# Optimization experiments

Hardware: AMD Instinct MI355X
Metric: run time of the kernel (lower is better)

Reference implementation:

```python
import jax, jax.numpy as jnp
import numpy as np

# MXFP4 e2m1 value lookup (sign bit is the high bit of the nibble)
FP4_LUT = jnp.array([0.0, 0.5, 1.0, 1.5, 2.0, 3.0, 4.0, 6.0,
                     -0.0, -0.5, -1.0, -1.5, -2.0, -3.0, -4.0, -6.0], dtype=jnp.float32)
BLOCK = 32  # mxfp4 scale block size
TOP_K = 2


def dequant_mxfp4(blocks, scales):
    # blocks: [..., K//2] packed uint8 nibbles (low nibble = even elem, high = odd)
    # scales: [..., K//BLOCK] e8m0 biased exponents; scale = 2**(s - 127)
    b = blocks.astype(jnp.int32)
    lo = b & 0xF
    hi = (b >> 4) & 0xF
    nib = jnp.stack([lo, hi], axis=-1).reshape(blocks.shape[:-1] + (blocks.shape[-1] * 2,))
    vals = FP4_LUT[nib]                                   # [..., K]
    s = jnp.exp2(scales.astype(jnp.float32) - 127.0)      # [..., K//BLOCK]
    s = jnp.repeat(s, BLOCK, axis=-1)                     # [..., K]
    return vals * s


def setup_inputs() -> dict:
    key = jax.random.key(0)
    ks = jax.random.split(key, 8)
    E, H, F, B, S = 16, 1024, 2048, 1, 128
    hidden_states = jax.random.normal(ks[0], (B, S, H), dtype=jnp.float32)
    router_w = jax.random.normal(ks[1], (E, H), dtype=jnp.float32) * 0.05
    blocks_gu = jax.random.randint(ks[2], (E, 2 * F, H // 2), 0, 256, dtype=jnp.int32)
    scales_gu = jax.random.randint(ks[3], (E, 2 * F, H // BLOCK), 118, 130, dtype=jnp.int32)
    bias_gu = jax.random.normal(ks[4], (E, 2 * F), dtype=jnp.float32) * 0.02
    blocks_down = jax.random.randint(ks[5], (E, H, F // 2), 0, 256, dtype=jnp.int32)
    scales_down = jax.random.randint(ks[6], (E, H, F // BLOCK), 118, 130, dtype=jnp.int32)
    bias_down = jax.random.normal(ks[7], (E, H), dtype=jnp.float32) * 0.02
    return {"hidden_states": hidden_states, "router_w": router_w,
            "bias_gu": bias_gu, "bias_down": bias_down,
            "blocks_gu": blocks_gu, "scales_gu": scales_gu,
            "blocks_down": blocks_down, "scales_down": scales_down}


def reference(hidden_states, router_w, bias_gu, bias_down,
              blocks_gu, scales_gu, blocks_down, scales_down):
    B, S, H = hidden_states.shape
    flat = hidden_states.reshape(-1, H)                   # [T, H]
    T = flat.shape[0]
    E = router_w.shape[0]

    # --- routing: topk_then_softmax (default softmax_order) ---
    logits = flat @ router_w.T                            # [T, E]
    top_vals, top_idx = jax.lax.top_k(logits, TOP_K)      # [T, K]
    weights = jax.nn.softmax(top_vals, axis=-1).astype(flat.dtype)
    combine = jnp.zeros((T, E), flat.dtype).at[jnp.arange(T)[:, None], top_idx].set(weights)

    # --- mxfp4 dequant of fused expert weights ---
    w_gu = dequant_mxfp4(blocks_gu, scales_gu)            # [E, 2F, H]
    w_down = dequant_mxfp4(blocks_down, scales_down)      # [E, H, F]

    # --- expert MLP (SwiGLU), combined with routing weights ---
    gu = jnp.einsum('th,eoh->eto', flat, w_gu) + bias_gu[:, None, :]   # [E, T, 2F]
    gate, up = jnp.split(gu, 2, axis=-1)
    h = jax.nn.silu(gate) * up                            # [E, T, F]
    y = jnp.einsum('etf,ehf->eth', h, w_down) + bias_down[:, None, :]  # [E, T, H]
    out = jnp.einsum('eth,te->th', y, combine)            # [T, H]
    return out.reshape(B, S, H)
```

## Files before the change

### kernel.cpp

```cpp
#include <hip/hip_runtime.h>
#include <hip/hip_fp16.h>
#include <math.h>

#define NE 16
#define HD 1024
#define FD 2048

typedef _Float16 half8 __attribute__((ext_vector_type(8)));
typedef float f32x4 __attribute__((ext_vector_type(4)));

#define TOPI_OFF 0
#define TOPW_OFF 256
#define CNT_OFF  512
#define PREF_OFF 528
#define SLOT_OFF 544
#define INVT_OFF 800
#define META_OFF 1056
#define TL1_OFF  1060
#define XH_OFF   4096
#define HBUF_OFF (XH_OFF + 131072)
#define Y_OFF    (HBUF_OFF + 262144)

union XI { int4 v; half8 h; };

__device__ __forceinline__ int fp4h(int nib) {
    int c = nib & 7;
    int v;
    if (c == 0) v = 0;
    else if (c == 1) v = 14 << 10;
    else v = (((c >> 1) + 14) << 10) | ((c & 1) << 9);
    v |= (nib & 8) << 12;
    return v;
}

__device__ __forceinline__ int dec2i(const int* lut, int byte, int sv) {
    int l = lut[byte & 255];
    __half2 p = *reinterpret_cast<const __half2*>(&l);
    __half2 sc = *reinterpret_cast<const __half2*>(&sv);
    __half2 r = __hmul2(p, sc);
    return *reinterpret_cast<int*>(&r);
}

__global__ void routing_kernel(const float* __restrict__ x, const float* __restrict__ rw,
                               int* __restrict__ top_idx, float* __restrict__ top_w) {
    int t = blockIdx.x;
    int tid = threadIdx.x;
    int e = tid >> 4, seg = tid & 15;
    const float* xr = x + t * HD + seg * 64;
    const float* wr = rw + e * HD + seg * 64;
    float p = 0.f;
    #pragma unroll 8
    for (int i = 0; i < 64; ++i) p += xr[i] * wr[i];
    __shared__ float part[16][16];
    __shared__ float logit[16];
    part[e][seg] = p;
    __syncthreads();
    if (tid < 16) {
        float s = 0.f;
        #pragma unroll
        for (int i = 0; i < 16; ++i) s += part[tid][i];
        logit[tid] = s;
    }
    __syncthreads();
    if (tid == 0) {
        int i0 = 0; float v0 = logit[0];
        #pragma unroll
        for (int i = 1; i < 16; ++i) { if (logit[i] > v0) { v0 = logit[i]; i0 = i; } }
        int i1 = -1; float v1 = -1e30f;
        #pragma unroll
        for (int i = 0; i < 16; ++i) { if (i != i0 && logit[i] > v1) { v1 = logit[i]; i1 = i; } }
        float w0 = 1.f / (1.f + expf(v1 - v0));
        float w1 = 1.f / (1.f + expf(v0 - v1));
        top_idx[t * 2]     = i0;  top_w[t * 2]     = w0;
        top_idx[t * 2 + 1] = i1;  top_w[t * 2 + 1] = w1;
    }
}

__global__ void build_kernel(const int* __restrict__ top_idx,
                             int* __restrict__ cnt, int* __restrict__ pref,
                             int* __restrict__ slot, int* __restrict__ invtok,
                             int* __restrict__ meta, int* __restrict__ tl1) {
    __shared__ int scnt[16], spref[16], scur[16];
    int tid = threadIdx.x;
    if (tid < 16) scnt[tid] = 0;
    __syncthreads();
    int e = top_idx[tid];
    atomicAdd(&scnt[e], 1);
    __syncthreads();
    if (tid == 0) {
        int s = 0;
        for (int i = 0; i < 16; ++i) { spref[i] = s; pref[i] = s; cnt[i] = scnt[i]; s += scnt[i]; }
        int m1 = 0;
        for (int i = 0; i < 16; ++i) {
            int ntile1 = (scnt[i] + 15) >> 4;
            for (int m = 0; m < ntile1; ++m) tl1[m1++] = (i << 8) | m;
        }
        meta[0] = m1;
    }
    if (tid < 16) scur[tid] = 0;
    __syncthreads();
    int pos = spref[e] + atomicAdd(&scur[e], 1);
    slot[tid] = pos;
    invtok[pos] = tid >> 1;
}

__global__ void gather_kernel(const float* __restrict__ x, const int* __restrict__ invtok,
                              _Float16* __restrict__ xh) {
    int slt = blockIdx.x;
    int t = invtok[slt];
    int i = threadIdx.x;
    float4 v = ((const float4*)(x + (long)t * HD))[i];
    union { _Float16 h[4]; int2 p; } o;
    o.h[0] = (_Float16)v.x; o.h[1] = (_Float16)v.y;
    o.h[2] = (_Float16)v.z; o.h[3] = (_Float16)v.w;
    ((int2*)(xh + (long)slt * HD))[i] = o.p;
}

__global__ __launch_bounds__(256) void gemm1_mfma(
    const _Float16* __restrict__ xh, const int* __restrict__ qblk,
    const int* __restrict__ qscl, const float* __restrict__ bias,
    const int* __restrict__ cnt, const int* __restrict__ pref,
    const int* __restrict__ meta, const int* __restrict__ tl1,
    _Float16* __restrict__ hbuf) {
    __shared__ int lut[256];
    __shared__ int4 Asb[128];
    __shared__ int4 Bsb[512];
    __shared__ float exch[4][64][4];
    int tid = threadIdx.x;
    lut[tid] = fp4h(tid & 15) | (fp4h(tid >> 4) << 16);
    int wave = tid >> 6, lane = tid & 63;
    int bl = lane & 15, kb4 = lane >> 4;
    int rloc = wave * 16 + bl;
    int rs = tid >> 2, kq = tid & 3;
    int tok = tid >> 3, ga = tid & 7;
    int nwork = meta[0] << 6;

    for (int w = blockIdx.x; w < nwork; w += gridDim.x) {
        int tile = tl1[w >> 6];
        int fc = w & 63;
        int e = tile >> 8, mt = tile & 255;
        int n = cnt[e];
        int nt = n - mt * 16; if (nt > 16) nt = 16;
        int base = pref[e];
        int t0 = base + mt * 16;
        int f0 = fc * 32;

        long rowg = (long)e * 4096 + ((rs < 32) ? (f0 + rs) : (2048 + f0 + rs - 32));
        const int4* wrow = (const int4*)(qblk + rowg * 512);
        const int* srow = qscl + rowg * 32;
        int tclamp = (tok < nt) ? tok : nt - 1;
        const int4* arow = (const int4*)xh + (long)(t0 + tclamp) * 128;

        f32x4 acc = {0.f, 0.f, 0.f, 0.f};
        for (int kb = 0; kb < 16; ++kb) {
            __syncthreads();
            if (tid < 128)
                Asb[tok * 8 + (ga ^ (tok & 7))] = arow[kb * 8 + ga];
            {
                int4 q0 = wrow[kb * 8 + kq * 2];
                int4 q1 = wrow[kb * 8 + kq * 2 + 1];
                int sc = srow[kb * 2 + (kq >> 1)];
                int sv = (sc - 112) << 10; sv |= sv << 16;
                int4 o0, o1;
                o0.x = dec2i(lut, q0.x, sv); o0.y = dec2i(lut, q0.y, sv);
                o0.z = dec2i(lut, q0.z, sv); o0.w = dec2i(lut, q0.w, sv);
                o1.x = dec2i(lut, q1.x, sv); o1.y = dec2i(lut, q1.y, sv);
                o1.z = dec2i(lut, q1.z, sv); o1.w = dec2i(lut, q1.w, sv);
                Bsb[rs * 8 + ((kq * 2) ^ (rs & 7))] = o0;
                Bsb[rs * 8 + ((kq * 2 + 1) ^ (rs & 7))] = o1;
            }
            __syncthreads();
            #pragma unroll
            for (int ks = 0; ks < 2; ++ks) {
                int g = ks * 4 + kb4;
                XI a, b;
                a.v = Asb[bl * 8 + (g ^ (bl & 7))];
                b.v = Bsb[rloc * 8 + (g ^ (rloc & 7))];
                acc = __builtin_amdgcn_mfma_f32_16x16x32_f16(a.h, b.h, acc, 0, 0, 0);
            }
        }
        #pragma unroll
        for (int i = 0; i < 4; ++i) exch[wave][lane][i] = acc[i];
        __syncthreads();
        int fl = tid & 31, wv = fl >> 4, col = fl & 15;
        float bg = bias[(long)e * 4096 + f0 + fl];
        float bu = bias[(long)e * 4096 + 2048 + f0 + fl];
        #pragma unroll
        for (int d = 0; d < 2; ++d) {
            int tk = (tid >> 5) + d * 8;
            int ln = ((tk >> 2) << 4) | col;
            int rg = tk & 3;
            float g = exch[wv][ln][rg] + bg;
            float u = exch[wv + 2][ln][rg] + bu;
            float h = (g / (1.f + expf(-g))) * u;
            if (tk < nt)
                hbuf[(long)(t0 + tk) * FD + f0 + fl] = (_Float16)(h * 0.0625f);
        }
    }
}

__global__ __launch_bounds__(256) void gemm2_mfma(
    const _Float16* __restrict__ hbuf, const int* __restrict__ qblk,
    const int* __restrict__ qscl, const float* __restrict__ bias,
    const int* __restrict__ cnt, const int* __restrict__ pref,
    const int* __restrict__ meta, const int* __restrict__ tl1,
    float* __restrict__ y) {
    __shared__ int lut[256];
    __shared__ int4 Asb[128];
    __shared__ int4 Bsb[512];
    int tid = threadIdx.x;
    lut[tid] = fp4h(tid & 15) | (fp4h(tid >> 4) << 16);
    int wave = tid >> 6, lane = tid & 63;
    int bl = lane & 15, kb4 = lane >> 4;
    int rloc = wave * 16 + bl;
    int rs = tid >> 2, kq = tid & 3;
    int tok = tid >> 3, ga = tid & 7;
    int nwork = meta[0] << 5;

    for (int w = blockIdx.x; w < nwork; w += gridDim.x) {
        int tile = tl1[w >> 5];
        int sub = w & 31;
        int hc = sub & 15, kh = sub >> 4;
        int e = tile >> 8, mt = tile & 255;
        int n = cnt[e];
        int nt = n - mt * 16; if (nt > 16) nt = 16;
        int base = pref[e];
        int t0 = base + mt * 16;
        int h0 = hc * 64;

        long rowg = (long)e * HD + h0 + rs;
        const int4* wrow = (const int4*)(qblk + rowg * 1024);
        const int* srow = qscl + rowg * 64;
        int tclamp = (tok < nt) ? tok : nt - 1;
        const int4* arow = (const int4*)hbuf + (long)(t0 + tclamp) * 256;
        int kb0 = kh * 16;

        f32x4 acc = {0.f, 0.f, 0.f, 0.f};
        for (int kb = 0; kb < 16; ++kb) {
            int kbb = kb0 + kb;
            __syncthreads();
            if (tid < 128)
                Asb[tok * 8 + (ga ^ (tok & 7))] = arow[kbb * 8 + ga];
            {
                int4 q0 = wrow[kbb * 8 + kq * 2];
                int4 q1 = wrow[kbb * 8 + kq * 2 + 1];
                int sc = srow[kbb * 2 + (kq >> 1)];
                int sv = (sc - 112) << 10; sv |= sv << 16;
                int4 o0, o1;
                o0.x = dec2i(lut, q0.x, sv); o0.y = dec2i(lut, q0.y, sv);
                o0.z = dec2i(lut, q0.z, sv); o0.w = dec2i(lut, q0.w, sv);
                o1.x = dec2i(lut, q1.x, sv); o1.y = dec2i(lut, q1.y, sv);
                o1.z = dec2i(lut, q1.z, sv); o1.w = dec2i(lut, q1.w, sv);
                Bsb[rs * 8 + ((kq * 2) ^ (rs & 7))] = o0;
                Bsb[rs * 8 + ((kq * 2 + 1) ^ (rs & 7))] = o1;
            }
            __syncthreads();
            #pragma unroll
            for (int ks = 0; ks < 2; ++ks) {
                int g = ks * 4 + kb4;
                XI a, b;
                a.v = Asb[bl * 8 + (g ^ (bl & 7))];
                b.v = Bsb[rloc * 8 + (g ^ (rloc & 7))];
                acc = __builtin_amdgcn_mfma_f32_16x16x32_f16(a.h, b.h, acc, 0, 0, 0);
            }
        }
        int hcol = h0 + wave * 16 + bl;
        float bv = (kh == 0) ? bias[(long)e * HD + hcol] : 0.f;
        #pragma unroll
        for (int r = 0; r < 4; ++r) {
            int row = kb4 * 4 + r;
            if (row < nt)
                atomicAdd(&y[(long)(t0 + row) * HD + hcol], acc[r] * 16.f + bv);
        }
    }
}

__global__ void combine_kernel(const float* __restrict__ y, const int* __restrict__ slot,
                               const float* __restrict__ topw, float* __restrict__ out) {
    int t = blockIdx.x;
    int i = threadIdx.x;
    int s0 = slot[2 * t], s1 = slot[2 * t + 1];
    float w0 = topw[2 * t], w1 = topw[2 * t + 1];
    float4 a = ((const float4*)(y + (long)s0 * HD))[i];
    float4 b = ((const float4*)(y + (long)s1 * HD))[i];
    float4 o;
    o.x = w0 * a.x + w1 * b.x;
    o.y = w0 * a.y + w1 * b.y;
    o.z = w0 * a.z + w1 * b.z;
    o.w = w0 * a.w + w1 * b.w;
    ((float4*)(out + (long)t * HD))[i] = o;
}

extern "C" void kernel_launch(void* const* d_in, const int* in_sizes, int n_in,
                              void* d_out, int out_size, void* d_ws, size_t ws_size,
                              hipStream_t stream) {
    const float* x          = (const float*)d_in[0];
    const float* rw         = (const float*)d_in[1];
    const float* bias_gu    = (const float*)d_in[2];
    const float* bias_down  = (const float*)d_in[3];
    const int*   blocks_gu  = (const int*)d_in[4];
    const int*   scales_gu  = (const int*)d_in[5];
    const int*   blocks_down= (const int*)d_in[6];
    const int*   scales_down= (const int*)d_in[7];
    float* out = (float*)d_out;
    int*   wsI = (int*)d_ws;
    float* wsF = (float*)d_ws;
    _Float16* xh   = (_Float16*)(wsI + XH_OFF);
    _Float16* hbuf = (_Float16*)(wsI + HBUF_OFF);
    float*    y    = wsF + Y_OFF;

    (void)hipMemsetAsync(y, 0, 256 * HD * sizeof(float), stream);
    routing_kernel<<<128, 256, 0, stream>>>(x, rw, wsI + TOPI_OFF, wsF + TOPW_OFF);
    build_kernel<<<1, 256, 0, stream>>>(wsI + TOPI_OFF, wsI + CNT_OFF, wsI + PREF_OFF,
                                        wsI + SLOT_OFF, wsI + INVT_OFF,
                                        wsI + META_OFF, wsI + TL1_OFF);
    gather_kernel<<<256, 256, 0, stream>>>(x, wsI + INVT_OFF, xh);
    gemm1_mfma<<<2048, 256, 0, stream>>>(xh, blocks_gu, scales_gu, bias_gu,
                                         wsI + CNT_OFF, wsI + PREF_OFF,
                                         wsI + META_OFF, wsI + TL1_OFF, hbuf);
    gemm2_mfma<<<1024, 256, 0, stream>>>(hbuf, blocks_down, scales_down, bias_down,
                                         wsI + CNT_OFF, wsI + PREF_OFF,
                                         wsI + META_OFF, wsI + TL1_OFF, y);
    combine_kernel<<<128, 256, 0, stream>>>(y, wsI + SLOT_OFF, wsF + TOPW_OFF, out);
}
```

Before: 67.93 us.

## Double-buffer LDS tiles in both GEMMs and replace atomics with split-K buffers

Both GEMM kernels now keep two shared-memory buffers. Global loads for the next K block are issued before the MFMAs on the current block, and only one barrier is left per iteration, so memory latency overlaps with compute. The gemm2 split-K halves write plain stores into two separate y buffers instead of doing atomicAdd into one. This removes the memset and the atomic traffic, at the cost of combine reading four rows per token instead of two. The added cost is twice the LDS and more registers, which may reduce occupancy.

```diff
diff --git a/kernel.cpp b/kernel.cpp
--- a/kernel.cpp
+++ b/kernel.cpp
@@ -19,7 +19,8 @@
 #define TL1_OFF  1060
 #define XH_OFF   4096
 #define HBUF_OFF (XH_OFF + 131072)
-#define Y_OFF    (HBUF_OFF + 262144)
+#define Y0_OFF   (HBUF_OFF + 262144)
+#define Y1_OFF   (Y0_OFF + 262144)
 
 union XI { int4 v; half8 h; };
 
@@ -123,8 +124,8 @@
     const int* __restrict__ meta, const int* __restrict__ tl1,
     _Float16* __restrict__ hbuf) {
     __shared__ int lut[256];
-    __shared__ int4 Asb[128];
-    __shared__ int4 Bsb[512];
+    __shared__ int4 Asb[2][128];
+    __shared__ int4 Bsb[2][512];
     __shared__ float exch[4][64][4];
     int tid = threadIdx.x;
     lut[tid] = fp4h(tid & 15) | (fp4h(tid >> 4) << 16);
@@ -151,32 +152,54 @@
         int tclamp = (tok < nt) ? tok : nt - 1;
         const int4* arow = (const int4*)xh + (long)(t0 + tclamp) * 128;
 
+        int4 q0 = wrow[kq * 2];
+        int4 q1 = wrow[kq * 2 + 1];
+        int sc = srow[kq >> 1];
+        int4 av;
+        if (tid < 128) av = arow[ga];
+        __syncthreads();
+        if (tid < 128) Asb[0][tok * 8 + (ga ^ (tok & 7))] = av;
+        {
+            int sv = (sc - 112) << 10; sv |= sv << 16;
+            int4 o0, o1;
+            o0.x = dec2i(lut, q0.x, sv); o0.y = dec2i(lut, q0.y, sv);
+            o0.z = dec2i(lut, q0.z, sv); o0.w = dec2i(lut, q0.w, sv);
+            o1.x = dec2i(lut, q1.x, sv); o1.y = dec2i(lut, q1.y, sv);
+            o1.z = dec2i(lut, q1.z, sv); o1.w = dec2i(lut, q1.w, sv);
+            Bsb[0][rs * 8 + ((kq * 2) ^ (rs & 7))] = o0;
+            Bsb[0][rs * 8 + ((kq * 2 + 1) ^ (rs & 7))] = o1;
+        }
+        __syncthreads();
+
         f32x4 acc = {0.f, 0.f, 0.f, 0.f};
         for (int kb = 0; kb < 16; ++kb) {
-            __syncthreads();
-            if (tid < 128)
-                Asb[tok * 8 + (ga ^ (tok & 7))] = arow[kb * 8 + ga];
-            {
-                int4 q0 = wrow[kb * 8 + kq * 2];
-                int4 q1 = wrow[kb * 8 + kq * 2 + 1];
-                int sc = srow[kb * 2 + (kq >> 1)];
+            int cur = kb & 1;
+            if (kb < 15) {
+                q0 = wrow[(kb + 1) * 8 + kq * 2];
+                q1 = wrow[(kb + 1) * 8 + kq * 2 + 1];
+                sc = srow[(kb + 1) * 2 + (kq >> 1)];
+                if (tid < 128) av = arow[(kb + 1) * 8 + ga];
+            }
+            #pragma unroll
+            for (int ks = 0; ks < 2; ++ks) {
+                int g = ks * 4 + kb4;
+                XI a, b;
+                a.v = Asb[cur][bl * 8 + (g ^ (bl & 7))];
+                b.v = Bsb[cur][rloc * 8 + (g ^ (rloc & 7))];
+                acc = __builtin_amdgcn_mfma_f32_16x16x32_f16(a.h, b.h, acc, 0, 0, 0);
+            }
+            if (kb < 15) {
+                int nxt = cur ^ 1;
+                if (tid < 128) Asb[nxt][tok * 8 + (ga ^ (tok & 7))] = av;
                 int sv = (sc - 112) << 10; sv |= sv << 16;
                 int4 o0, o1;
                 o0.x = dec2i(lut, q0.x, sv); o0.y = dec2i(lut, q0.y, sv);
                 o0.z = dec2i(lut, q0.z, sv); o0.w = dec2i(lut, q0.w, sv);
                 o1.x = dec2i(lut, q1.x, sv); o1.y = dec2i(lut, q1.y, sv);
                 o1.z = dec2i(lut, q1.z, sv); o1.w = dec2i(lut, q1.w, sv);
-                Bsb[rs * 8 + ((kq * 2) ^ (rs & 7))] = o0;
-                Bsb[rs * 8 + ((kq * 2 + 1) ^ (rs & 7))] = o1;
-            }
-            __syncthreads();
-            #pragma unroll
-            for (int ks = 0; ks < 2; ++ks) {
-                int g = ks * 4 + kb4;
-                XI a, b;
-                a.v = Asb[bl * 8 + (g ^ (bl & 7))];
-                b.v = Bsb[rloc * 8 + (g ^ (rloc & 7))];
-                acc = __builtin_amdgcn_mfma_f32_16x16x32_f16(a.h, b.h, acc, 0, 0, 0);
+                Bsb[nxt][rs * 8 + ((kq * 2) ^ (rs & 7))] = o0;
+                Bsb[nxt][rs * 8 + ((kq * 2 + 1) ^ (rs & 7))] = o1;
+                __syncthreads();
             }
         }
         #pragma unroll
@@ -204,10 +227,10 @@
     const int* __restrict__ qscl, const float* __restrict__ bias,
     const int* __restrict__ cnt, const int* __restrict__ pref,
     const int* __restrict__ meta, const int* __restrict__ tl1,
-    float* __restrict__ y) {
+    float* __restrict__ y0p, float* __restrict__ y1p) {
     __shared__ int lut[256];
-    __shared__ int4 Asb[128];
-    __shared__ int4 Bsb[512];
+    __shared__ int4 Asb[2][128];
+    __shared__ int4 Bsb[2][512];
     int tid = threadIdx.x;
     lut[tid] = fp4h(tid & 15) | (fp4h(tid >> 4) << 16);
     int wave = tid >> 6, lane = tid & 63;
@@ -229,65 +252,90 @@
         int h0 = hc * 64;
 
         long rowg = (long)e * HD + h0 + rs;
-        const int4* wrow = (const int4*)(qblk + rowg * 1024);
-        const int* srow = qscl + rowg * 64;
+        const int4* wrow = (const int4*)(qblk + rowg * 1024) + (kh * 16) * 8;
+        const int* srow = qscl + rowg * 64 + kh * 32;
         int tclamp = (tok < nt) ? tok : nt - 1;
-        const int4* arow = (const int4*)hbuf + (long)(t0 + tclamp) * 256;
-        int kb0 = kh * 16;
+        const int4* arow = (const int4*)hbuf + (long)(t0 + tclamp) * 256 + (kh * 16) * 8;
+
+        int4 q0 = wrow[kq * 2];
+        int4 q1 = wrow[kq * 2 + 1];
+        int sc = srow[kq >> 1];
+        int4 av;
+        if (tid < 128) av = arow[ga];
+        __syncthreads();
+        if (tid < 128) Asb[0][tok * 8 + (ga ^ (tok & 7))] = av;
+        {
+            int sv = (sc - 112) << 10; sv |= sv << 16;
+            int4 o0, o1;
+            o0.x = dec2i(lut, q0.x, sv); o0.y = dec2i(lut, q0.y, sv);
+            o0.z = dec2i(lut, q0.z, sv); o0.w = dec2i(lut, q0.w, sv);
+            o1.x = dec2i(lut, q1.x, sv); o1.y = dec2i(lut, q1.y, sv);
+            o1.z = dec2i(lut, q1.z, sv); o1.w = dec2i(lut, q1.w, sv);
+            Bsb[0][rs * 8 + ((kq * 2) ^ (rs & 7))] = o0;
+            Bsb[0][rs * 8 + ((kq * 2 + 1) ^ (rs & 7))] = o1;
+        }
+        __syncthreads();
 
         f32x4 acc = {0.f, 0.f, 0.f, 0.f};
         for (int kb = 0; kb < 16; ++kb) {
-            int kbb = kb0 + kb;
-            __syncthreads();
-            if (tid < 128)
-                Asb[tok * 8 + (ga ^ (tok & 7))] = arow[kbb * 8 + ga];
-            {
-                int4 q0 = wrow[kbb * 8 + kq * 2];
-                int4 q1 = wrow[kbb * 8 + kq * 2 + 1];
-                int sc = srow[kbb * 2 + (kq >> 1)];
+            int cur = kb & 1;
+            if (kb < 15) {
+                q0 = wrow[(kb + 1) * 8 + kq * 2];
+                q1 = wrow[(kb + 1) * 8 + kq * 2 + 1];
+                sc = srow[(kb + 1) * 2 + (kq >> 1)];
+                if (tid < 128) av = arow[(kb + 1) * 8 + ga];
+            }
+            #pragma unroll
+            for (int ks = 0; ks < 2; ++ks) {
+                int g = ks * 4 + kb4;
+                XI a, b;
+                a.v = Asb[cur][bl * 8 + (g ^ (bl & 7))];
+                b.v = Bsb[cur][rloc * 8 + (g ^ (rloc & 7))];
+                acc = __builtin_amdgcn_mfma_f32_16x16x32_f16(a.h, b.h, acc, 0, 0, 0);
+            }
+            if (kb < 15) {
+                int nxt = cur ^ 1;
+                if (tid < 128) Asb[nxt][tok * 8 + (ga ^ (tok & 7))] = av;
                 int sv = (sc - 112) << 10; sv |= sv << 16;
                 int4 o0, o1;
                 o0.x = dec2i(lut, q0.x, sv); o0.y = dec2i(lut, q0.y, sv);
                 o0.z = dec2i(lut, q0.z, sv); o0.w = dec2i(lut, q0.w, sv);
                 o1.x = dec2i(lut, q1.x, sv); o1.y = dec2i(lut, q1.y, sv);
                 o1.z = dec2i(lut, q1.z, sv); o1.w = dec2i(lut, q1.w, sv);
-                Bsb[rs * 8 + ((kq * 2) ^ (rs & 7))] = o0;
-                Bsb[rs * 8 + ((kq * 2 + 1) ^ (rs & 7))] = o1;
-            }
-            __syncthreads();
-            #pragma unroll
-            for (int ks = 0; ks < 2; ++ks) {
-                int g = ks * 4 + kb4;
-                XI a, b;
-                a.v = Asb[bl * 8 + (g ^ (bl & 7))];
-                b.v = Bsb[rloc * 8 + (g ^ (rloc & 7))];
-                acc = __builtin_amdgcn_mfma_f32_16x16x32_f16(a.h, b.h, acc, 0, 0, 0);
+                Bsb[nxt][rs * 8 + ((kq * 2) ^ (rs & 7))] = o0;
+                Bsb[nxt][rs * 8 + ((kq * 2 + 1) ^ (rs & 7))] = o1;
+                __syncthreads();
             }
         }
         int hcol = h0 + wave * 16 + bl;
         float bv = (kh == 0) ? bias[(long)e * HD + hcol] : 0.f;
+        float* yp = (kh == 0) ? y0p : y1p;
         #pragma unroll
         for (int r = 0; r < 4; ++r) {
             int row = kb4 * 4 + r;
             if (row < nt)
-                atomicAdd(&y[(long)(t0 + row) * HD + hcol], acc[r] * 16.f + bv);
-        }
-    }
-}
-
-__global__ void combine_kernel(const float* __restrict__ y, const int* __restrict__ slot,
-                               const float* __restrict__ topw, float* __restrict__ out) {
+                yp[(long)(t0 + row) * HD + hcol] = acc[r] * 16.f + bv;
+        }
+        __syncthreads();
+    }
+}
+
+__global__ void combine_kernel(const float* __restrict__ y0, const float* __restrict__ y1,
+                               const int* __restrict__ slot, const float* __restrict__ topw,
+                               float* __restrict__ out) {
     int t = blockIdx.x;
     int i = threadIdx.x;
     int s0 = slot[2 * t], s1 = slot[2 * t + 1];
     float w0 = topw[2 * t], w1 = topw[2 * t + 1];
-    float4 a = ((const float4*)(y + (long)s0 * HD))[i];
-    float4 b = ((const float4*)(y + (long)s1 * HD))[i];
+    float4 a0 = ((const float4*)(y0 + (long)s0 * HD))[i];
+    float4 a1 = ((const float4*)(y1 + (long)s0 * HD))[i];
+    float4 b0 = ((const float4*)(y0 + (long)s1 * HD))[i];
+    float4 b1 = ((const float4*)(y1 + (long)s1 * HD))[i];
     float4 o;
-    o.x = w0 * a.x + w1 * b.x;
-    o.y = w0 * a.y + w1 * b.y;
-    o.z = w0 * a.z + w1 * b.z;
-    o.w = w0 * a.w + w1 * b.w;
+    o.x = w0 * (a0.x + a1.x) + w1 * (b0.x + b1.x);
+    o.y = w0 * (a0.y + a1.y) + w1 * (b0.y + b1.y);
+    o.z = w0 * (a0.z + a1.z) + w1 * (b0.z + b1.z);
+    o.w = w0 * (a0.w + a1.w) + w1 * (b0.w + b1.w);
     ((float4*)(out + (long)t * HD))[i] = o;
 }
 
@@ -307,9 +355,9 @@
     float* wsF = (float*)d_ws;
     _Float16* xh   = (_Float16*)(wsI + XH_OFF);
     _Float16* hbuf = (_Float16*)(wsI + HBUF_OFF);
-    float*    y    = wsF + Y_OFF;
-
-    (void)hipMemsetAsync(y, 0, 256 * HD * sizeof(float), stream);
+    float*    y0   = wsF + Y0_OFF;
+    float*    y1   = wsF + Y1_OFF;
+
     routing_kernel<<<128, 256, 0, stream>>>(x, rw, wsI + TOPI_OFF, wsF + TOPW_OFF);
     build_kernel<<<1, 256, 0, stream>>>(wsI + TOPI_OFF, wsI + CNT_OFF, wsI + PREF_OFF,
                                         wsI + SLOT_OFF, wsI + INVT_OFF,
@@ -320,6 +368,6 @@
                                          wsI + META_OFF, wsI + TL1_OFF, hbuf);
     gemm2_mfma<<<1024, 256, 0, stream>>>(hbuf, blocks_down, scales_down, bias_down,
                                          wsI + CNT_OFF, wsI + PREF_OFF,
-                                         wsI + META_OFF, wsI + TL1_OFF, y);
-    combine_kernel<<<128, 256, 0, stream>>>(y, wsI + SLOT_OFF, wsF + TOPW_OFF, out);
-}
+                                         wsI + META_OFF, wsI + TL1_OFF, y0, y1);
+    combine_kernel<<<128, 256, 0, stream>>>(y0, y1, wsI + SLOT_OFF, wsF + TOPW_OFF, out);
+}
```

Result: faster. 60.87 us (-10.4%).
